# Kernel optimization log

Measured on AMD Instinct MI355X. Metric: run time of the kernel, lower is better.

The kernel has to match this reference:

```python
import jax, jax.numpy as jnp
import numpy as np

B, TQ, TK = 4, 1024, 1024
D, H, DFF = 1024, 16, 4096
DH = D // H
EPS = 1e-6  # added to sigma (std), not variance, per the torch LayerNorm


def layer_norm(x, g, b):
    mu = jnp.mean(x, axis=-1, keepdims=True)
    sigma = jnp.sqrt(jnp.mean((x - mu) ** 2, axis=-1, keepdims=True))  # unbiased=False
    return (x - mu) / (sigma + EPS) * g + b


def mha(q_in, k_in, v_in, mask, wq, bq, wk, bk, wv, bv, wo, bo):
    # q_in: [B,Tq,D], k_in/v_in: [B,Tk,D], mask: [B,Tq,Tk] bool (True = masked)
    b, tq, _ = q_in.shape
    tk = k_in.shape[1]
    q = (q_in @ wq + bq).reshape(b, tq, H, DH).transpose(0, 2, 1, 3)  # [B,H,Tq,DH]
    k = (k_in @ wk + bk).reshape(b, tk, H, DH).transpose(0, 2, 1, 3)  # [B,H,Tk,DH]
    v = (v_in @ wv + bv).reshape(b, tk, H, DH).transpose(0, 2, 1, 3)  # [B,H,Tk,DH]
    logits = jnp.einsum('bhqd,bhkd->bhqk', q, k) / np.float32(np.sqrt(DH))
    logits = jnp.where(mask[:, None, :, :], -jnp.inf, logits)  # broadcast over heads
    attn = jax.nn.softmax(logits, axis=-1)
    out = jnp.einsum('bhqk,bhkd->bhqd', attn, v)  # [B,H,Tq,DH]
    out = out.transpose(0, 2, 1, 3).reshape(b, tq, D)  # [B,Tq,D]
    return out @ wo + bo


def setup_inputs() -> dict:
    key = jax.random.key(0)
    ks = jax.random.split(key, 32)
    s = 0.02
    def lin(i, din, dout):
        return (jax.random.normal(ks[i], (din, dout), jnp.float32) * s,
                jnp.zeros((dout,), jnp.float32))
    inp = {}
    inp['x'] = jax.random.normal(ks[0], (B, TQ, D), jnp.float32)
    inp['src_x'] = jax.random.normal(ks[1], (B, TK, D), jnp.float32)
    causal = jnp.triu(jnp.ones((TQ, TQ), jnp.bool_), k=1)
    inp['mask'] = jnp.broadcast_to(causal, (B, TQ, TQ))
    inp['src_mask'] = jnp.zeros((B, TQ, TK), jnp.bool_)
    for j, (g, bname) in enumerate([('ln1_g', 'ln1_b'), ('ln2_g', 'ln2_b'), ('ln3_g', 'ln3_b')]):
        inp[g] = jnp.ones((D,), jnp.float32)
        inp[bname] = jnp.zeros((D,), jnp.float32)
    names = ['sa_wq', 'sa_wk', 'sa_wv', 'sa_wo', 'ca_wq', 'ca_wk', 'ca_wv', 'ca_wo']
    for j, n in enumerate(names):
        w, bb = lin(2 + j, D, D)
        inp[n] = w
        inp[n.replace('w', 'b', 1).replace('_b', '_b')] = bb
        inp[n[:3] + 'b' + n[4]] = bb
    # clean bias naming
    for n in names:
        inp.pop(n[:3] + 'b' + n[4], None)
        inp.pop(n.replace('w', 'b', 1), None)
    for j, n in enumerate(names):
        w, bb = lin(2 + j, D, D)
        inp[n] = w
        inp['b' + n] = bb
    w1, b1 = lin(12, D, DFF)
    w2, b2 = lin(13, DFF, D)
    inp['ff_w1'], inp['ff_b1'], inp['ff_w2'], inp['ff_b2'] = w1, b1, w2, b2
    return inp


def reference(x, src_x, mask, src_mask,
              ln1_g, ln1_b, ln2_g, ln2_b, ln3_g, ln3_b,
              sa_wq, bsa_wq, sa_wk, bsa_wk, sa_wv, bsa_wv, sa_wo, bsa_wo,
              ca_wq, bca_wq, ca_wk, bca_wk, ca_wv, bca_wv, ca_wo, bca_wo,
              ff_w1, ff_b1, ff_w2, ff_b2):
    # pre-layer-norm decoder layer (dropout=0 / eval mode)
    h = layer_norm(x, ln1_g, ln1_b)
    x1 = x + mha(h, h, h, mask, sa_wq, bsa_wq, sa_wk, bsa_wk, sa_wv, bsa_wv, sa_wo, bsa_wo)
    h2 = layer_norm(x1, ln2_g, ln2_b)
    x2 = x1 + mha(h2, src_x, src_x, src_mask, ca_wq, bca_wq, ca_wk, bca_wk, ca_wv, bca_wv, ca_wo, bca_wo)
    h3 = layer_norm(x2, ln3_g, ln3_b)
    ff = jax.nn.relu(h3 @ ff_w1 + ff_b1) @ ff_w2 + ff_b2
    return x2 + ff
```

## Files before the change

### kernel.cpp

```cpp
#include <hip/hip_runtime.h>

typedef __bf16 bf16;
typedef __attribute__((ext_vector_type(8))) __bf16 bf16x8;
typedef __attribute__((ext_vector_type(4))) __bf16 bf16x4;
typedef __attribute__((ext_vector_type(4))) float f32x4;

#define MFMA16(a, b, c) __builtin_amdgcn_mfma_f32_16x16x32_bf16((a), (b), (c), 0, 0, 0)

static const long MMe = 1L << 20;
#define QSCALE_F 0.18033688011112042f

__device__ __forceinline__ void async_cp16(void* lds, const void* g) {
    __builtin_amdgcn_global_load_lds((__attribute__((address_space(1))) void*)g,
                                     (__attribute__((address_space(3))) void*)lds, 16, 0, 0);
}

__global__ __launch_bounds__(256) void cvt_k(const float* __restrict__ in,
                                             bf16* __restrict__ out)
{
    const long i = (long)blockIdx.x * 1024 + threadIdx.x * 4;
    f32x4 v = *(const f32x4*)(in + i);
    bf16x4 o;
    for (int j = 0; j < 4; ++j) o[j] = (bf16)v[j];
    *(bf16x4*)(out + i) = o;
}

__global__ __launch_bounds__(256) void ln_k(const float* __restrict__ x,
                                            const float* __restrict__ g,
                                            const float* __restrict__ b,
                                            bf16* __restrict__ out)
{
    __shared__ float red1[4];
    __shared__ float red2[4];
    const int tid  = threadIdx.x;
    const int wave = tid >> 6, lane = tid & 63;
    const long row = blockIdx.x;

    f32x4 v = *(const f32x4*)(x + row * 1024 + tid * 4);
    float s = v[0] + v[1] + v[2] + v[3];
    for (int off = 32; off > 0; off >>= 1) s += __shfl_xor(s, off, 64);
    if (lane == 0) red1[wave] = s;
    __syncthreads();
    const float mu = (red1[0] + red1[1] + red1[2] + red1[3]) * (1.f / 1024.f);

    float s2 = 0.f;
    for (int i = 0; i < 4; ++i) { float d = v[i] - mu; s2 += d * d; }
    for (int off = 32; off > 0; off >>= 1) s2 += __shfl_xor(s2, off, 64);
    if (lane == 0) red2[wave] = s2;
    __syncthreads();
    const float var = (red2[0] + red2[1] + red2[2] + red2[3]) * (1.f / 1024.f);
    const float inv = 1.f / (sqrtf(var) + 1e-6f);

    f32x4 gv = *(const f32x4*)(g + tid * 4);
    f32x4 bv = *(const f32x4*)(b + tid * 4);
    bf16x4 ov;
    for (int i = 0; i < 4; ++i)
        ov[i] = (bf16)((v[i] - mu) * inv * gv[i] + bv[i]);
    *(bf16x4*)(out + row * 1024 + tid * 4) = ov;
}

__global__ __launch_bounds__(256) void transpose8_k(
    const float* i0, const float* i1, const float* i2, const float* i3,
    const float* i4, const float* i5, const float* i6, const float* i7,
    bf16* outB)
{
    __shared__ bf16 t[32][33];
    const float* in;
    switch (blockIdx.z) {
        case 0: in = i0; break; case 1: in = i1; break;
        case 2: in = i2; break; case 3: in = i3; break;
        case 4: in = i4; break; case 5: in = i5; break;
        case 6: in = i6; break; default: in = i7; break;
    }
    bf16* out = outB + ((long)blockIdx.z << 20);
    const int bx = blockIdx.x * 32, by = blockIdx.y * 32;
    const int r = threadIdx.x >> 5, c = threadIdx.x & 31;
    for (int i = 0; i < 4; ++i)
        t[r + i * 8][c] = (bf16)in[(long)(by + r + i * 8) * 1024 + bx + c];
    __syncthreads();
    for (int i = 0; i < 4; ++i)
        out[(long)(bx + r + i * 8) * 1024 + by + c] = t[c][r + i * 8];
}

__global__ __launch_bounds__(256) void transpose_k(const float* __restrict__ in,
                                                   bf16* __restrict__ out, int R, int C)
{
    __shared__ bf16 t[32][33];
    const int bx = blockIdx.x * 32, by = blockIdx.y * 32;
    const int r = threadIdx.x >> 5, c = threadIdx.x & 31;
    for (int i = 0; i < 4; ++i)
        t[r + i * 8][c] = (bf16)in[(long)(by + r + i * 8) * C + bx + c];
    __syncthreads();
    for (int i = 0; i < 4; ++i)
        out[(long)(bx + r + i * 8) * R + by + c] = t[c][r + i * 8];
}

template <int BM, int BN, int STORE, bool BIAS, bool RELU, bool RES, bool OUTF32, bool SPLIT, bool QS, bool DUALA, int PX>
__global__ __launch_bounds__(256) void gemm_k(const bf16* __restrict__ A,
                                              const bf16* __restrict__ A2,
                                              int lda,
                                              const bf16* __restrict__ Bt, int ldb,
                                              const float* __restrict__ bias,
                                              const float* __restrict__ bias2,
                                              const float* __restrict__ bias3,
                                              const float* __restrict__ res,
                                              void* __restrict__ Cv,
                                              void* __restrict__ Cv2,
                                              int M, int N, int K)
{
    constexpr int MI = BM / 32, NI = BN / 32;
    __shared__ __align__(16) bf16 As[BM * 64];
    __shared__ __align__(16) bf16 Bs[BN * 64];
    const int tid  = threadIdx.x;
    const int wave = tid >> 6, lane = tid & 63;
    const int quad = lane >> 4, l15 = lane & 15;
    const int wm = wave >> 1, wn = wave & 1;

    int tx, ty, tz;
    if (PX > 0) {
        const unsigned wgid = (blockIdx.z * gridDim.y + blockIdx.y) * gridDim.x + blockIdx.x;
        const int xcd = wgid & 7, lid = wgid >> 3;
        const int npx = gridDim.x / PX;
        const int PY  = (gridDim.y * gridDim.z) / (8 / npx);
        const int ix  = lid % PX, iyz = lid / PX;
        const int pxi = xcd % npx, pyi = xcd / npx;
        const int tyz = pyi * PY + iyz;
        tx = pxi * PX + ix;
        ty = tyz % gridDim.y;
        tz = tyz / gridDim.y;
    } else {
        tx = blockIdx.x; ty = blockIdx.y; tz = blockIdx.z;
    }

    const long m0 = (long)ty * BM;
    const long n0 = (long)tx * BN;
    const long kbase = SPLIT ? (long)tz * K : 0;

    const bf16* Abase = A;
    if (DUALA && (n0 >> 10) >= 1) Abase = A2;

    f32x4 acc[MI][NI];
    for (int i = 0; i < MI; ++i)
        for (int j = 0; j < NI; ++j)
            acc[i][j] = (f32x4){0.f, 0.f, 0.f, 0.f};

    const int lr = lane >> 3;
    const int lc = (((lane & 7) ^ (lr & 7)) * 8);
    const bf16* Ag = Abase + (m0 + lr) * (long)lda + lc + kbase;
    const bf16* Bg = Bt    + (n0 + lr) * (long)ldb + lc + kbase;

    for (int k0 = 0; k0 < K; k0 += 64) {
        __syncthreads();
        for (int s = wave; s < BM / 8; s += 4)
            async_cp16(&As[s * 512], Ag + (long)(s * 8) * lda + k0);
        for (int s = wave; s < BN / 8; s += 4)
            async_cp16(&Bs[s * 512], Bg + (long)(s * 8) * ldb + k0);
        __syncthreads();
        for (int kk = 0; kk < 2; ++kk) {
            bf16x8 af[MI], bfr[NI];
            for (int i = 0; i < MI; ++i) {
                const int row = wm * (BM / 2) + i * 16 + l15;
                af[i]  = *(const bf16x8*)&As[row * 64 + (((kk * 4 + quad) ^ (l15 & 7)) * 8)];
            }
            for (int j = 0; j < NI; ++j) {
                const int row = wn * (BN / 2) + j * 16 + l15;
                bfr[j] = *(const bf16x8*)&Bs[row * 64 + (((kk * 4 + quad) ^ (l15 & 7)) * 8)];
            }
            for (int mi = 0; mi < MI; ++mi)
                for (int ni = 0; ni < NI; ++ni)
                    acc[mi][ni] = MFMA16(af[mi], bfr[ni], acc[mi][ni]);
        }
    }

    float* outp = (float*)Cv;
    if (SPLIT && tz) outp = (float*)Cv2;

    for (int ni = 0; ni < NI; ++ni) {
        const int col = (int)n0 + wn * (BN / 2) + ni * 16 + l15;
        float bv = 0.f;
        int which = 0, c1 = col;
        if (STORE == 3) {
            which = col >> 10; c1 = col & 1023;
            if (BIAS) bv = (which == 0 ? bias : (which == 1 ? bias2 : bias3))[c1];
        } else if (STORE == 4) {
            which = col >> 10; c1 = col & 1023;
            if (BIAS) bv = (which ? bias2 : bias)[c1];
        } else if (BIAS) {
            bv = bias[col];
        }
        for (int mi = 0; mi < MI; ++mi) {
            for (int r = 0; r < 4; ++r) {
                const int row = (int)m0 + wm * (BM / 2) + mi * 16 + quad * 4 + r;
                float v = acc[mi][ni][r] + bv;
                if (QS && (STORE == 1 || (STORE == 3 && which == 0))) v *= QSCALE_F;
                if (RES)  v += res[(long)row * N + col];
                if (RELU) v = v > 0.f ? v : 0.f;
                long oidx;
                if (STORE == 0) {
                    oidx = (long)row * N + col;
                } else {
                    const int bb = row >> 10, t = row & 1023;
                    const int hh = c1 >> 6,  dh = c1 & 63;
                    const long qidx = ((long)(bb * 16 + hh) * 1024 + t) * 64 + dh;
                    const long vidx = ((long)(bb * 16 + hh) * 64 + dh) * 1024 + t;
                    if (STORE == 1)      oidx = qidx;
                    else if (STORE == 2) oidx = vidx;
                    else if (STORE == 3) oidx = (which == 2) ? (8 * MMe + vidx)
                                                             : ((long)which * 4 * MMe + qidx);
                    else                 oidx = which ? (4 * MMe + vidx) : qidx;
                }
                if (OUTF32) outp[oidx] = v;
                else        ((bf16*)Cv)[oidx] = (bf16)v;
            }
        }
    }
}

__global__ __launch_bounds__(256) void red2_k(const float* __restrict__ P0,
                                              const float* __restrict__ P1,
                                              const float* __restrict__ bias,
                                              const float* __restrict__ res,
                                              float* __restrict__ out)
{
    const long i = (long)blockIdx.x * 1024 + threadIdx.x * 4;
    f32x4 a = *(const f32x4*)(P0 + i);
    f32x4 b = *(const f32x4*)(P1 + i);
    f32x4 r = *(const f32x4*)(res + i);
    f32x4 bv = *(const f32x4*)(bias + threadIdx.x * 4);
    f32x4 o;
    for (int j = 0; j < 4; ++j) o[j] = a[j] + b[j] + r[j] + bv[j];
    *(f32x4*)(out + i) = o;
}

__device__ __forceinline__ void attn_tile(const bf16x8* aq,
                                          const bf16* Ks, const bf16* Vs, bf16* Psw,
                                          int tk0, int q0w, int quad, int l15, int l7,
                                          bool domask, f32x4* o, float* rs)
{
    f32x4 s[8];
    for (int ct = 0; ct < 8; ++ct) {
        f32x4 sv = (f32x4){0.f, 0.f, 0.f, 0.f};
        sv = MFMA16(aq[0], *(const bf16x8*)&Ks[(ct * 16 + l15) * 64 + ((quad ^ l7) * 8)], sv);
        sv = MFMA16(aq[1], *(const bf16x8*)&Ks[(ct * 16 + l15) * 64 + (((4 + quad) ^ l7) * 8)], sv);
        s[ct] = sv;
    }
    if (domask) {
        for (int ct = 0; ct < 8; ++ct) {
            const int cg = tk0 + ct * 16 + l15;
            for (int r = 0; r < 4; ++r)
                if (cg > q0w + quad * 4 + r) s[ct][r] = -1e30f;
        }
    }
    for (int ct = 0; ct < 8; ++ct) {
        for (int r = 0; r < 4; ++r) {
            const float p = exp2f(s[ct][r]);
            rs[r] += p;
            Psw[(quad * 4 + r) * 136 + ct * 16 + l15] = (bf16)p;
        }
    }
    for (int kk = 0; kk < 4; ++kk) {
        const bf16x8 ap = *(const bf16x8*)&Psw[l15 * 136 + kk * 32 + quad * 8];
        for (int nt = 0; nt < 4; ++nt) {
            const bf16x8 bv = *(const bf16x8*)&Vs[(nt * 16 + l15) * 128 + (((kk * 4 + quad) ^ l15) * 8)];
            o[nt] = MFMA16(ap, bv, o[nt]);
        }
    }
}

__global__ __launch_bounds__(256) void attn_causal_k(const bf16* __restrict__ Q,
                                                     const bf16* __restrict__ K,
                                                     const bf16* __restrict__ Vt,
                                                     bf16* __restrict__ Out)
{
    __shared__ __align__(16) bf16 Ks[128 * 64];
    __shared__ __align__(16) bf16 Vs[64 * 128];
    __shared__ __align__(16) bf16 Ps[4][16 * 136];

    const int tid  = threadIdx.x;
    const int wave = tid >> 6, lane = tid & 63;
    const int quad = lane >> 4, l15 = lane & 15, l7 = l15 & 7;
    const int x  = blockIdx.x;
    const int bh = blockIdx.y;
    const int hh = bh & 15, bb = bh >> 4;

    const bf16* Qp = Q  + (long)bh * 1024 * 64;
    const bf16* Kp = K  + (long)bh * 1024 * 64;
    const bf16* Vp = Vt + (long)bh * 64 * 1024;

    const int qA = x, qB = 15 - x;
    const int q0A = qA * 64 + wave * 16, q0B = qB * 64 + wave * 16;
    const int chA = qA >> 1, chB = qB >> 1;

    bf16x8 aqA[2], aqB[2];
    aqA[0] = *(const bf16x8*)&Qp[(q0A + l15) * 64 + quad * 8];
    aqA[1] = *(const bf16x8*)&Qp[(q0A + l15) * 64 + quad * 8 + 32];
    aqB[0] = *(const bf16x8*)&Qp[(q0B + l15) * 64 + quad * 8];
    aqB[1] = *(const bf16x8*)&Qp[(q0B + l15) * 64 + quad * 8 + 32];

    f32x4 oA[4], oB[4];
    float rsA[4] = {0.f, 0.f, 0.f, 0.f}, rsB[4] = {0.f, 0.f, 0.f, 0.f};
    for (int nt = 0; nt < 4; ++nt) {
        oA[nt] = (f32x4){0.f, 0.f, 0.f, 0.f};
        oB[nt] = (f32x4){0.f, 0.f, 0.f, 0.f};
    }

    const int krow = lane >> 3;
    const int kcol = (((lane & 7) ^ (krow & 7)) * 8);
    const int vrow = lane >> 4;

    for (int ch = 0; ch <= chB; ++ch) {
        const int tk0 = ch * 128;
        __syncthreads();
        for (int s = wave; s < 16; s += 4)
            async_cp16(&Ks[s * 512], &Kp[(long)(tk0 + s * 8 + krow) * 64 + kcol]);
        for (int s = wave; s < 16; s += 4) {
            const int row = s * 4 + vrow;
            const int vcol = ((l15 ^ (row & 15)) * 8);
            async_cp16(&Vs[s * 512], &Vp[(long)row * 1024 + tk0 + vcol]);
        }
        __syncthreads();
        if (ch <= chA)
            attn_tile(aqA, Ks, Vs, Ps[wave], tk0, q0A, quad, l15, l7, ch == chA, oA, rsA);
        attn_tile(aqB, Ks, Vs, Ps[wave], tk0, q0B, quad, l15, l7, ch == chB, oB, rsB);
    }

    for (int r = 0; r < 4; ++r) {
        for (int off = 1; off < 16; off <<= 1) {
            rsA[r] += __shfl_xor(rsA[r], off, 64);
            rsB[r] += __shfl_xor(rsB[r], off, 64);
        }
    }
    for (int nt = 0; nt < 4; ++nt) {
        for (int r = 0; r < 4; ++r) {
            const int col = hh * 64 + nt * 16 + l15;
            Out[((long)bb * 1024 + q0A + quad * 4 + r) * 1024 + col] = (bf16)(oA[nt][r] / rsA[r]);
            Out[((long)bb * 1024 + q0B + quad * 4 + r) * 1024 + col] = (bf16)(oB[nt][r] / rsB[r]);
        }
    }
}

__global__ __launch_bounds__(256) void attn_cross_k(const bf16* __restrict__ Q,
                                                    const bf16* __restrict__ K,
                                                    const bf16* __restrict__ Vt,
                                                    bf16* __restrict__ Out)
{
    __shared__ __align__(16) bf16 Ks[128 * 64];
    __shared__ __align__(16) bf16 Vs[64 * 128];
    __shared__ __align__(16) bf16 Ps[4][16 * 136];

    const int tid  = threadIdx.x;
    const int wave = tid >> 6, lane = tid & 63;
    const int quad = lane >> 4, l15 = lane & 15, l7 = l15 & 7;
    const int qb = blockIdx.x;
    const int bh = blockIdx.y;
    const int hh = bh & 15, bb = bh >> 4;

    const bf16* Qp = Q  + (long)bh * 1024 * 64;
    const bf16* Kp = K  + (long)bh * 1024 * 64;
    const bf16* Vp = Vt + (long)bh * 64 * 1024;
    const int q0w = qb * 64 + wave * 16;

    bf16x8 aq[2];
    aq[0] = *(const bf16x8*)&Qp[(q0w + l15) * 64 + quad * 8];
    aq[1] = *(const bf16x8*)&Qp[(q0w + l15) * 64 + quad * 8 + 32];

    f32x4 o[4];
    float rs[4] = {0.f, 0.f, 0.f, 0.f};
    for (int nt = 0; nt < 4; ++nt) o[nt] = (f32x4){0.f, 0.f, 0.f, 0.f};

    const int krow = lane >> 3;
    const int kcol = (((lane & 7) ^ (krow & 7)) * 8);
    const int vrow = lane >> 4;

    for (int ch = 0; ch < 8; ++ch) {
        const int tk0 = ch * 128;
        __syncthreads();
        for (int s = wave; s < 16; s += 4)
            async_cp16(&Ks[s * 512], &Kp[(long)(tk0 + s * 8 + krow) * 64 + kcol]);
        for (int s = wave; s < 16; s += 4) {
            const int row = s * 4 + vrow;
            const int vcol = ((l15 ^ (row & 15)) * 8);
            async_cp16(&Vs[s * 512], &Vp[(long)row * 1024 + tk0 + vcol]);
        }
        __syncthreads();
        attn_tile(aq, Ks, Vs, Ps[wave], tk0, q0w, quad, l15, l7, false, o, rs);
    }

    for (int r = 0; r < 4; ++r)
        for (int off = 1; off < 16; off <<= 1) rs[r] += __shfl_xor(rs[r], off, 64);

    for (int nt = 0; nt < 4; ++nt) {
        for (int r = 0; r < 4; ++r) {
            const int t   = q0w + quad * 4 + r;
            const int col = hh * 64 + nt * 16 + l15;
            Out[((long)bb * 1024 + t) * 1024 + col] = (bf16)(o[nt][r] / rs[r]);
        }
    }
}

extern "C" void kernel_launch(void* const* d_in, const int* in_sizes, int n_in,
                              void* d_out, int out_size, void* d_ws, size_t ws_size,
                              hipStream_t stream)
{
    const float* x     = (const float*)d_in[0];
    const float* src_x = (const float*)d_in[1];
    const float* ln1_g = (const float*)d_in[4];
    const float* ln1_b = (const float*)d_in[5];
    const float* ln2_g = (const float*)d_in[6];
    const float* ln2_b = (const float*)d_in[7];
    const float* ln3_g = (const float*)d_in[8];
    const float* ln3_b = (const float*)d_in[9];
    const float* sa_wq = (const float*)d_in[10];
    const float* sa_wk = (const float*)d_in[11];
    const float* sa_wv = (const float*)d_in[12];
    const float* sa_wo = (const float*)d_in[13];
    const float* ca_wq = (const float*)d_in[14];
    const float* ca_wk = (const float*)d_in[15];
    const float* ca_wv = (const float*)d_in[16];
    const float* ca_wo = (const float*)d_in[17];
    const float* bsa_wq = (const float*)d_in[18];
    const float* bsa_wk = (const float*)d_in[19];
    const float* bsa_wv = (const float*)d_in[20];
    const float* bsa_wo = (const float*)d_in[21];
    const float* bca_wq = (const float*)d_in[22];
    const float* bca_wk = (const float*)d_in[23];
    const float* bca_wv = (const float*)d_in[24];
    const float* bca_wo = (const float*)d_in[25];
    const float* ff_w1 = (const float*)d_in[26];
    const float* ff_b1 = (const float*)d_in[27];
    const float* ff_w2 = (const float*)d_in[28];
    const float* ff_b2 = (const float*)d_in[29];

    bf16* ws = (bf16*)d_ws;
    bf16*  WT_SA = ws;
    bf16*  WT_CA = ws + 4 * MMe;
    bf16*  WT_F1 = ws + 8 * MMe;
    bf16*  WT_F2 = ws + 12 * MMe;
    bf16*  Hbuf  = ws + 16 * MMe;
    bf16*  SrcB  = ws + 20 * MMe;
    bf16*  Qb    = ws + 24 * MMe;
    bf16*  Kb    = ws + 28 * MMe;
    bf16*  Vtb   = ws + 32 * MMe;
    bf16*  Attn  = ws + 36 * MMe;
    float* X1    = (float*)(ws + 40 * MMe);
    bf16*  FF1   = ws + 24 * MMe;
    float* P0    = (float*)ws;
    float* P1    = (float*)(ws + 16 * MMe);
    float* X2    = (float*)d_out;

    const dim3 blk(256);

    transpose8_k<<<dim3(32, 32, 8), blk, 0, stream>>>(sa_wq, sa_wk, sa_wv, sa_wo,
                                                      ca_wq, ca_wk, ca_wv, ca_wo, WT_SA);
    transpose_k<<<dim3(128, 32), blk, 0, stream>>>(ff_w1, WT_F1, 1024, 4096);
    transpose_k<<<dim3(32, 128), blk, 0, stream>>>(ff_w2, WT_F2, 4096, 1024);
    cvt_k<<<4096, blk, 0, stream>>>(src_x, SrcB);

    ln_k<<<4096, blk, 0, stream>>>(x, ln1_g, ln1_b, Hbuf);
    gemm_k<128, 128, 3, true, false, false, false, false, true, false, 6><<<dim3(24, 32), blk, 0, stream>>>(
        Hbuf, nullptr, 1024, WT_SA, 1024, bsa_wq, bsa_wk, bsa_wv, nullptr, Qb, nullptr, 4096, 3072, 1024);
    attn_causal_k<<<dim3(8, 64), blk, 0, stream>>>(Qb, Kb, Vtb, Attn);
    gemm_k<64, 128, 0, true, false, true, true, false, false, false, 8><<<dim3(8, 64), blk, 0, stream>>>(
        Attn, nullptr, 1024, WT_SA + 3 * MMe, 1024, bsa_wo, nullptr, nullptr, x, X1, nullptr, 4096, 1024, 1024);

    ln_k<<<4096, blk, 0, stream>>>(X1, ln2_g, ln2_b, Hbuf);
    gemm_k<64, 128, 3, true, false, false, false, false, true, true, 6><<<dim3(24, 64), blk, 0, stream>>>(
        Hbuf, SrcB, 1024, WT_CA, 1024, bca_wq, bca_wk, bca_wv, nullptr, Qb, nullptr, 4096, 3072, 1024);
    attn_cross_k<<<dim3(16, 64), blk, 0, stream>>>(Qb, Kb, Vtb, Attn);
    gemm_k<64, 128, 0, true, false, true, true, false, false, false, 8><<<dim3(8, 64), blk, 0, stream>>>(
        Attn, nullptr, 1024, WT_CA + 3 * MMe, 1024, bca_wo, nullptr, nullptr, X1, X2, nullptr, 4096, 1024, 1024);

    ln_k<<<4096, blk, 0, stream>>>(X2, ln3_g, ln3_b, Hbuf);
    gemm_k<128, 128, 0, true, true, false, false, false, false, false, 8><<<dim3(32, 32), blk, 0, stream>>>(
        Hbuf, nullptr, 1024, WT_F1, 1024, ff_b1, nullptr, nullptr, nullptr, FF1, nullptr, 4096, 4096, 1024);
    gemm_k<128, 128, 0, false, false, false, true, true, false, false, 8><<<dim3(8, 32, 2), blk, 0, stream>>>(
        FF1, nullptr, 4096, WT_F2, 4096, nullptr, nullptr, nullptr, nullptr, P0, P1, 4096, 1024, 2048);
    red2_k<<<4096, blk, 0, stream>>>(P0, P1, ff_b2, X2, (float*)d_out);

    (void)in_sizes; (void)n_in; (void)out_size; (void)ws_size;
}
```

Baseline: 528.3 us.

## Add 256x256-tile 512-thread GEMM kernel for QKV and FFN1 projections

Introduces a new GEMM kernel with 256x256 output tiles, 8 waves, double-buffered async global-to-LDS loads, swizzled LDS layout, and interleaved staging of the next K-tile between MFMA phases. It replaces the 128x128/64x128 GEMMs for the self- and cross-attention QKV projections and the first FFN matmul. The larger tile raises arithmetic intensity and cuts global/L2 traffic. In exchange it launches fewer workgroups (192 or 256), which may underfill the 256 CUs, and uses 128KB of LDS per block.

```diff
diff --git a/kernel.cpp b/kernel.cpp
--- a/kernel.cpp
+++ b/kernel.cpp
@@ -93,6 +93,165 @@
     __syncthreads();
     for (int i = 0; i < 4; ++i)
         out[(long)(bx + r + i * 8) * R + by + c] = t[c][r + i * 8];
+}
+
+template <int STORE, bool BIAS, bool RELU, bool QS, bool DUALA, int PX>
+__global__ __launch_bounds__(512, 2) void gemm256_k(
+    const bf16* __restrict__ A, const bf16* __restrict__ A2, int lda,
+    const bf16* __restrict__ Bt, int ldb,
+    const float* __restrict__ bias,
+    const float* __restrict__ bias2,
+    const float* __restrict__ bias3,
+    bf16* __restrict__ C, int N, int K)
+{
+    __shared__ __align__(16) bf16 As[2][256 * 64];
+    __shared__ __align__(16) bf16 Bs[2][256 * 64];
+    const int tid  = threadIdx.x;
+    const int wave = tid >> 6, lane = tid & 63;
+    const int quad = lane >> 4, l15 = lane & 15;
+    const int wm = wave >> 2, wn = wave & 3;
+
+    int tx, ty;
+    {
+        const unsigned wgid = blockIdx.y * gridDim.x + blockIdx.x;
+        const int xcd = wgid & 7, lid = wgid >> 3;
+        const int npx = gridDim.x / PX;
+        const int PY  = gridDim.y / (8 / npx);
+        const int ix  = lid % PX, iy = lid / PX;
+        const int pxi = xcd % npx, pyi = xcd / npx;
+        tx = pxi * PX + ix;
+        ty = pyi * PY + iy;
+    }
+    const long m0 = (long)ty * 256;
+    const long n0 = (long)tx * 256;
+    const bf16* Abase = A;
+    if (DUALA && (n0 >> 10) >= 1) Abase = A2;
+
+    f32x4 acc[8][4];
+    #pragma unroll
+    for (int i = 0; i < 8; ++i)
+        #pragma unroll
+        for (int j = 0; j < 4; ++j)
+            acc[i][j] = (f32x4){0.f, 0.f, 0.f, 0.f};
+
+    const int lr = lane >> 3;
+    const int lc = (((lane & 7) ^ (lr & 7)) * 8);
+    const bf16* Ag = Abase + (m0 + wave * 8 + lr) * (long)lda + lc;
+    const bf16* Bg = Bt    + (n0 + wave * 8 + lr) * (long)ldb + lc;
+    const int NT = K >> 6;
+
+#define STAGE_A256(buf, kt) { _Pragma("unroll") \
+    for (int a = 0; a < 4; ++a) \
+        async_cp16(&As[buf][(a * 64 + wave * 8) * 64], Ag + (long)(a * 64) * lda + (kt) * 64); }
+#define STAGE_B256(buf, kt) { _Pragma("unroll") \
+    for (int a = 0; a < 4; ++a) \
+        async_cp16(&Bs[buf][(a * 64 + wave * 8) * 64], Bg + (long)(a * 64) * ldb + (kt) * 64); }
+
+    STAGE_A256(0, 0); STAGE_B256(0, 0);
+    STAGE_A256(1, 1); STAGE_B256(1, 1);
+    asm volatile("s_waitcnt vmcnt(8)" ::: "memory");
+    __builtin_amdgcn_s_barrier();
+
+    for (int t = 0; t < NT; ++t) {
+        const int c = t & 1;
+        bf16x8 bfr[4][2];
+        bf16x8 af[2][2];
+
+        #pragma unroll
+        for (int ni = 0; ni < 4; ++ni)
+            #pragma unroll
+            for (int kk = 0; kk < 2; ++kk)
+                bfr[ni][kk] = *(const bf16x8*)&Bs[c][(wn * 64 + ni * 16 + l15) * 64 +
+                                                     (((kk * 4 + quad) ^ (l15 & 7)) * 8)];
+        #pragma unroll
+        for (int j = 0; j < 2; ++j)
+            #pragma unroll
+            for (int kk = 0; kk < 2; ++kk)
+                af[j][kk] = *(const bf16x8*)&As[c][(wm * 128 + j * 16 + l15) * 64 +
+                                                   (((kk * 4 + quad) ^ (l15 & 7)) * 8)];
+        __builtin_amdgcn_s_barrier();
+        asm volatile("s_waitcnt lgkmcnt(0)" ::: "memory");
+        __builtin_amdgcn_sched_barrier(0);
+        __builtin_amdgcn_s_setprio(1);
+        #pragma unroll
+        for (int j = 0; j < 2; ++j)
+            #pragma unroll
+            for (int ni = 0; ni < 4; ++ni)
+                #pragma unroll
+                for (int kk = 0; kk < 2; ++kk)
+                    acc[j][ni] = MFMA16(af[j][kk], bfr[ni][kk], acc[j][ni]);
+        __builtin_amdgcn_s_setprio(0);
+        __builtin_amdgcn_s_barrier();
+
+        #pragma unroll
+        for (int p = 1; p < 4; ++p) {
+            if (p == 1 && t + 2 < NT) STAGE_B256(c, t + 2);
+            #pragma unroll
+            for (int j = 0; j < 2; ++j)
+                #pragma unroll
+                for (int kk = 0; kk < 2; ++kk)
+                    af[j][kk] = *(const bf16x8*)&As[c][(wm * 128 + (2 * p + j) * 16 + l15) * 64 +
+                                                       (((kk * 4 + quad) ^ (l15 & 7)) * 8)];
+            __builtin_amdgcn_s_barrier();
+            asm volatile("s_waitcnt lgkmcnt(0)" ::: "memory");
+            __builtin_amdgcn_sched_barrier(0);
+            __builtin_amdgcn_s_setprio(1);
+            #pragma unroll
+            for (int j = 0; j < 2; ++j)
+                #pragma unroll
+                for (int ni = 0; ni < 4; ++ni)
+                    #pragma unroll
+                    for (int kk = 0; kk < 2; ++kk)
+                        acc[2 * p + j][ni] = MFMA16(af[j][kk], bfr[ni][kk], acc[2 * p + j][ni]);
+            __builtin_amdgcn_s_setprio(0);
+            __builtin_amdgcn_s_barrier();
+        }
+
+        if (t + 2 < NT) {
+            STAGE_A256(c, t + 2);
+            asm volatile("s_waitcnt vmcnt(8)" ::: "memory");
+            __builtin_amdgcn_s_barrier();
+        } else if (t + 1 < NT) {
+            asm volatile("s_waitcnt vmcnt(0)" ::: "memory");
+            __builtin_amdgcn_s_barrier();
+        }
+    }
+#undef STAGE_A256
+#undef STAGE_B256
+
+    #pragma unroll
+    for (int ni = 0; ni < 4; ++ni) {
+        const int col = (int)n0 + wn * 64 + ni * 16 + l15;
+        float bv = 0.f;
+        int which = 0, c1 = col;
+        if (STORE == 3) {
+            which = col >> 10; c1 = col & 1023;
+            if (BIAS) bv = (which == 0 ? bias : (which == 1 ? bias2 : bias3))[c1];
+        } else if (BIAS) {
+            bv = bias[col];
+        }
+        #pragma unroll
+        for (int mi = 0; mi < 8; ++mi) {
+            #pragma unroll
+            for (int r = 0; r < 4; ++r) {
+                const int row = (int)m0 + wm * 128 + mi * 16 + quad * 4 + r;
+                float v = acc[mi][ni][r] + bv;
+                if (QS && STORE == 3 && which == 0) v *= QSCALE_F;
+                if (RELU) v = v > 0.f ? v : 0.f;
+                long oidx;
+                if (STORE == 0) {
+                    oidx = (long)row * N + col;
+                } else {
+                    const int bb = row >> 10, tt = row & 1023;
+                    const int hh = c1 >> 6,  dh = c1 & 63;
+                    const long qidx = ((long)(bb * 16 + hh) * 1024 + tt) * 64 + dh;
+                    const long vidx = ((long)(bb * 16 + hh) * 64 + dh) * 1024 + tt;
+                    oidx = (which == 2) ? (8 * MMe + vidx) : ((long)which * 4 * MMe + qidx);
+                }
+                C[oidx] = (bf16)v;
+            }
+        }
+    }
 }
 
 template <int BM, int BN, int STORE, bool BIAS, bool RELU, bool RES, bool OUTF32, bool SPLIT, bool QS, bool DUALA, int PX>
@@ -449,6 +608,7 @@
     float* X2    = (float*)d_out;
 
     const dim3 blk(256);
+    const dim3 blk512(512);
 
     transpose8_k<<<dim3(32, 32, 8), blk, 0, stream>>>(sa_wq, sa_wk, sa_wv, sa_wo,
                                                       ca_wq, ca_wk, ca_wv, ca_wo, WT_SA);
@@ -457,22 +617,22 @@
     cvt_k<<<4096, blk, 0, stream>>>(src_x, SrcB);
 
     ln_k<<<4096, blk, 0, stream>>>(x, ln1_g, ln1_b, Hbuf);
-    gemm_k<128, 128, 3, true, false, false, false, false, true, false, 6><<<dim3(24, 32), blk, 0, stream>>>(
-        Hbuf, nullptr, 1024, WT_SA, 1024, bsa_wq, bsa_wk, bsa_wv, nullptr, Qb, nullptr, 4096, 3072, 1024);
+    gemm256_k<3, true, false, true, false, 3><<<dim3(12, 16), blk512, 0, stream>>>(
+        Hbuf, nullptr, 1024, WT_SA, 1024, bsa_wq, bsa_wk, bsa_wv, Qb, 3072, 1024);
     attn_causal_k<<<dim3(8, 64), blk, 0, stream>>>(Qb, Kb, Vtb, Attn);
     gemm_k<64, 128, 0, true, false, true, true, false, false, false, 8><<<dim3(8, 64), blk, 0, stream>>>(
         Attn, nullptr, 1024, WT_SA + 3 * MMe, 1024, bsa_wo, nullptr, nullptr, x, X1, nullptr, 4096, 1024, 1024);
 
     ln_k<<<4096, blk, 0, stream>>>(X1, ln2_g, ln2_b, Hbuf);
-    gemm_k<64, 128, 3, true, false, false, false, false, true, true, 6><<<dim3(24, 64), blk, 0, stream>>>(
-        Hbuf, SrcB, 1024, WT_CA, 1024, bca_wq, bca_wk, bca_wv, nullptr, Qb, nullptr, 4096, 3072, 1024);
+    gemm256_k<3, true, false, true, true, 3><<<dim3(12, 16), blk512, 0, stream>>>(
+        Hbuf, SrcB, 1024, WT_CA, 1024, bca_wq, bca_wk, bca_wv, Qb, 3072, 1024);
     attn_cross_k<<<dim3(16, 64), blk, 0, stream>>>(Qb, Kb, Vtb, Attn);
     gemm_k<64, 128, 0, true, false, true, true, false, false, false, 8><<<dim3(8, 64), blk, 0, stream>>>(
         Attn, nullptr, 1024, WT_CA + 3 * MMe, 1024, bca_wo, nullptr, nullptr, X1, X2, nullptr, 4096, 1024, 1024);
 
     ln_k<<<4096, blk, 0, stream>>>(X2, ln3_g, ln3_b, Hbuf);
-    gemm_k<128, 128, 0, true, true, false, false, false, false, false, 8><<<dim3(32, 32), blk, 0, stream>>>(
-        Hbuf, nullptr, 1024, WT_F1, 1024, ff_b1, nullptr, nullptr, nullptr, FF1, nullptr, 4096, 4096, 1024);
+    gemm256_k<0, true, true, false, false, 2><<<dim3(16, 16), blk512, 0, stream>>>(
+        Hbuf, nullptr, 1024, WT_F1, 1024, ff_b1, nullptr, nullptr, FF1, 4096, 1024);
     gemm_k<128, 128, 0, false, false, false, true, true, false, false, 8><<<dim3(8, 32, 2), blk, 0, stream>>>(
         FF1, nullptr, 4096, WT_F2, 4096, nullptr, nullptr, nullptr, nullptr, P0, P1, 4096, 1024, 2048);
     red2_k<<<4096, blk, 0, stream>>>(P0, P1, ff_b2, X2, (float*)d_out);
```

Result: slower. 565.1 us (+7.0%).
